# Performance work log

Hardware: AMD Instinct MI355X
Metric: run time of the kernel (lower is better)

## Reference

```python
import jax, jax.numpy as jnp
import numpy as np

B, S, D = 16, 4096, 128
LN_EPS = 1e-5
REC_EPS = 1e-8


def setup_inputs() -> dict:
    key = jax.random.key(0)
    k1, k2, k3, k4 = jax.random.split(key, 4)
    return {
        "C": jax.random.normal(k1, (B, S, D), dtype=jnp.float32),
        "V": jax.random.normal(k2, (B, S, D), dtype=jnp.float32),
        "W": jax.random.normal(k3, (B, S, D), dtype=jnp.float32),
        "encoder_context": jax.random.normal(k4, (B, D), dtype=jnp.float32),
        "time_modulation": jnp.full((1, 1, D), 0.5, dtype=jnp.float32),
        "context_modulation": jnp.full((1, D), 0.5, dtype=jnp.float32),
        "ln_weight": jnp.ones((D,), dtype=jnp.float32),
        "ln_bias": jnp.zeros((D,), dtype=jnp.float32),
    }


def reference(C, V, W, encoder_context, time_modulation, context_modulation, ln_weight, ln_bias):
    b_, s_, d_ = C.shape
    tm = time_modulation[0, 0]  # [D]
    # context gate is time-invariant: compute once
    ctx_add = jax.nn.sigmoid(encoder_context * context_modulation) * encoder_context  # [B,D]

    def step(carry, xs):
        a, bst = carry  # a: [B,1], bst: [B,D]
        c_t, v_t, w_t = xs  # each [B,D]
        decay = jax.nn.sigmoid(w_t * tm)  # [B,D]
        ec = jnp.exp(c_t)  # [B,D]
        a = decay.mean(axis=1, keepdims=True) * a + ec.sum(axis=1, keepdims=True)
        bst = decay * bst + ec * v_t + ctx_add
        out_t = bst / (a + REC_EPS)
        return (a, bst), out_t

    a0 = jnp.zeros((b_, 1), dtype=C.dtype)
    b0 = jnp.zeros((b_, d_), dtype=C.dtype)
    xs = (jnp.swapaxes(C, 0, 1), jnp.swapaxes(V, 0, 1), jnp.swapaxes(W, 0, 1))  # [S,B,D]
    _, ys = jax.lax.scan(step, (a0, b0), xs)  # ys: [S,B,D]
    res = jnp.swapaxes(ys, 0, 1)  # [B,S,D]

    mu = jnp.mean(res, axis=-1, keepdims=True)
    var = jnp.var(res, axis=-1, keepdims=True)
    normed = (res - mu) * jax.lax.rsqrt(var + LN_EPS)
    return normed * ln_weight + ln_bias
```

## Files before the change

### kernel.cpp

```cpp
#include <hip/hip_runtime.h>

#define BB   16
#define SS   4096
#define DD   128
#define NCH  256
#define TT   (SS / NCH)
#define WPB  4
#define NTHR 256

#define DT   16
#define SUBS 16
#define CPS  (NCH / SUBS)

#define LN_EPS  1e-5f
#define REC_EPS 1e-8f

__device__ __forceinline__ float fast_rcp(float x) { return __builtin_amdgcn_rcpf(x); }
__device__ __forceinline__ float sigm(float x) { return fast_rcp(1.0f + __expf(-x)); }

__device__ __forceinline__ unsigned pack2(float a, float b) {
    unsigned ua = (__float_as_uint(a) + 0x8000u) >> 16;
    unsigned ub = (__float_as_uint(b) + 0x8000u) & 0xFFFF0000u;
    return ub | ua;
}
__device__ __forceinline__ float up_lo(unsigned u) { return __uint_as_float(u << 16); }
__device__ __forceinline__ float up_hi(unsigned u) { return __uint_as_float(u & 0xFFFF0000u); }

template<int CTRL>
__device__ __forceinline__ float dpp_mov0(float x) {
    return __int_as_float(
        __builtin_amdgcn_update_dpp(0, __float_as_int(x), CTRL, 0xF, 0xF, true));
}

__device__ __forceinline__ void wave_red2(float& a, float& b) {
    a += dpp_mov0<0x111>(a); b += dpp_mov0<0x111>(b);
    a += dpp_mov0<0x112>(a); b += dpp_mov0<0x112>(b);
    a += dpp_mov0<0x114>(a); b += dpp_mov0<0x114>(b);
    a += dpp_mov0<0x118>(a); b += dpp_mov0<0x118>(b);
    a += dpp_mov0<0x142>(a); b += dpp_mov0<0x142>(b);
    a += dpp_mov0<0x143>(a); b += dpp_mov0<0x143>(b);
    a = __int_as_float(__builtin_amdgcn_readlane(__float_as_int(a), 63));
    b = __int_as_float(__builtin_amdgcn_readlane(__float_as_int(b), 63));
}

#define LOAD_FENCE() asm volatile("" ::: "memory")

__global__ __launch_bounds__(NTHR, 2) void pass1_kernel(
    const float* __restrict__ C, const float* __restrict__ V, const float* __restrict__ W,
    const float* __restrict__ enc, const float* __restrict__ tmod, const float* __restrict__ cmod,
    unsigned* __restrict__ DTb,
    float* __restrict__ Pbuf, float* __restrict__ Qbuf,
    float* __restrict__ PaBuf, float* __restrict__ QaBuf,
    float2* __restrict__ MEbuf)
{
    const int wv   = threadIdx.x >> 6;
    const int lane = threadIdx.x & 63;
    const int gc   = blockIdx.x * WPB + wv;
    const int b    = gc >> 8;
    const int ch   = gc & (NCH - 1);
    const int d2   = lane << 1;

    const int t0 = ch * TT;
    const size_t base = ((size_t)b * SS + t0) * DD + d2;
    const float2* Cp = (const float2*)(C + base);
    const float2* Vp = (const float2*)(V + base);
    const float2* Wp = (const float2*)(W + base);
    uint2* DTp = (uint2*)(DTb + base);

    const float2 tm = *(const float2*)(tmod + d2);
    const float2 cm = *(const float2*)(cmod + d2);
    const float2 ec = *(const float2*)(enc + b * DD + d2);

    float2 cR[TT], wR[TT], vR[TT];
#pragma unroll
    for (int t = 0; t < TT; ++t) {
        cR[t] = Cp[t * (DD / 2)];
        wR[t] = Wp[t * (DD / 2)];
        vR[t] = Vp[t * (DD / 2)];
    }
    LOAD_FENCE();

    float2 ctx;
    ctx.x = sigm(ec.x * cm.x) * ec.x;
    ctx.y = sigm(ec.y * cm.y) * ec.y;

    float2 P = make_float2(1.f, 1.f);
    float2 Q = make_float2(0.f, 0.f);
    float pa = 1.f, qa = 0.f;
    float mkeep = 0.f, ekeep = 0.f;

#pragma unroll
    for (int t = 0; t < TT; ++t) {
        float2 dec, e2, T2;
        dec.x = sigm(wR[t].x * tm.x); dec.y = sigm(wR[t].y * tm.y);
        e2.x = __expf(cR[t].x); e2.y = __expf(cR[t].y);
        T2.x = e2.x * vR[t].x + ctx.x;
        T2.y = e2.y * vR[t].y + ctx.y;

        uint2 u;
        u.x = pack2(dec.x, T2.x); u.y = pack2(dec.y, T2.y);
        DTp[t * (DD / 2)] = u;

        const float dqx = up_lo(u.x), dqy = up_lo(u.y);
        const float tqx = up_hi(u.x), tqy = up_hi(u.y);
        Q.x = dqx * Q.x + tqx;
        Q.y = dqy * Q.y + tqy;
        P.x *= dqx; P.y *= dqy;

        float sd = dec.x + dec.y;
        float se = e2.x + e2.y;
        wave_red2(sd, se);
        const float mt = sd * (1.0f / DD);
        pa *= mt;
        qa = mt * qa + se;
        if (lane == t) { mkeep = mt; ekeep = se; }
    }

    *(float2*)(Pbuf + (size_t)gc * DD + d2) = P;
    *(float2*)(Qbuf + (size_t)gc * DD + d2) = Q;
    if (lane < TT) MEbuf[(size_t)b * SS + t0 + lane] = make_float2(mkeep, ekeep);
    if (lane == 0) { PaBuf[gc] = pa; QaBuf[gc] = qa; }
}

__global__ __launch_bounds__(256) void pass2_kernel(
    const float* __restrict__ Pbuf, const float* __restrict__ Qbuf,
    const float* __restrict__ PaBuf, const float* __restrict__ QaBuf,
    float* __restrict__ bst0, float* __restrict__ a0)
{
    const int b   = blockIdx.x >> 3;
    const int dt  = blockIdx.x & 7;
    const int tid = threadIdx.x;
    const int dl  = tid & (DT - 1);
    const int sub = tid >> 4;
    const int d   = dt * DT + dl;

    __shared__ float cP[SUBS][DT], cQ[SUBS][DT], ent[SUBS][DT];
    __shared__ float sPa[NCH], sQa[NCH];

    const int ch0 = sub * CPS;
    const size_t base = ((size_t)b * NCH + ch0) * DD + d;
    float Pr[CPS], Qr[CPS];
    float p = 1.f, q = 0.f;
#pragma unroll
    for (int i = 0; i < CPS; ++i) {
        Pr[i] = Pbuf[base + (size_t)i * DD];
        Qr[i] = Qbuf[base + (size_t)i * DD];
        q = Pr[i] * q + Qr[i];
        p = Pr[i] * p;
    }
    cP[sub][dl] = p; cQ[sub][dl] = q;
    __syncthreads();

    if (tid < DT) {
        float s = 0.f;
#pragma unroll
        for (int sb = 0; sb < SUBS; ++sb) {
            ent[sb][tid] = s;
            s = cP[sb][tid] * s + cQ[sb][tid];
        }
    }
    __syncthreads();

    float s = ent[sub][dl];
#pragma unroll
    for (int i = 0; i < CPS; ++i) {
        bst0[base + (size_t)i * DD] = s;
        s = Pr[i] * s + Qr[i];
    }

    if (dt == 0) {
        float pa = PaBuf[b * NCH + tid];
        float qa = QaBuf[b * NCH + tid];
#pragma unroll
        for (int off = 1; off < NCH; off <<= 1) {
            sPa[tid] = pa; sQa[tid] = qa;
            __syncthreads();
            if (tid >= off) {
                const float pp = sPa[tid - off], qq = sQa[tid - off];
                qa = pa * qq + qa;
                pa = pa * pp;
            }
            __syncthreads();
        }
        sQa[tid] = qa;
        __syncthreads();
        a0[b * NCH + tid] = (tid == 0) ? 0.f : sQa[tid - 1];
    }
}

__global__ __launch_bounds__(NTHR, 4) void pass3_kernel(
    const unsigned* __restrict__ DTb,
    const float* __restrict__ lnw, const float* __restrict__ lnb,
    const float* __restrict__ bst0, const float* __restrict__ a0,
    const float2* __restrict__ MEbuf,
    float* __restrict__ out)
{
    const int wv   = threadIdx.x >> 6;
    const int lane = threadIdx.x & 63;
    const int gc   = blockIdx.x * WPB + wv;
    const int b    = gc >> 8;
    const int ch   = gc & (NCH - 1);
    const int d2   = lane << 1;

    const int t0 = ch * TT;
    const size_t base = ((size_t)b * SS + t0) * DD + d2;
    const uint2* DTp = (const uint2*)(DTb + base);
    float2* Op = (float2*)(out + base);

    uint2 dtR[TT];
#pragma unroll
    for (int t = 0; t < TT; ++t) dtR[t] = DTp[t * (DD / 2)];
    const float2 me = MEbuf[(size_t)b * SS + t0 + (lane & (TT - 1))];
    float2 bst = *(const float2*)(bst0 + (size_t)gc * DD + d2);
    const float a_in = a0[gc];
    const float2 gw = *(const float2*)(lnw + d2);
    const float2 gb = *(const float2*)(lnb + d2);
    LOAD_FENCE();

    float a = a_in;

#pragma unroll
    for (int t = 0; t < TT; ++t) {
        const float mt = __int_as_float(__builtin_amdgcn_readlane(__float_as_int(me.x), t));
        const float et = __int_as_float(__builtin_amdgcn_readlane(__float_as_int(me.y), t));

        a = mt * a + et;
        bst.x = up_lo(dtR[t].x) * bst.x + up_hi(dtR[t].x);
        bst.y = up_lo(dtR[t].y) * bst.y + up_hi(dtR[t].y);

        const float inva = fast_rcp(a + REC_EPS);
        float2 o;
        o.x = bst.x * inva; o.y = bst.y * inva;

        float s1 = o.x + o.y;
        float s2 = o.x * o.x + o.y * o.y;
        wave_red2(s1, s2);
        const float mu  = s1 * (1.0f / DD);
        const float var = s2 * (1.0f / DD) - mu * mu;
        const float rs  = rsqrtf(var + LN_EPS);

        float2 r;
        r.x = (o.x - mu) * rs * gw.x + gb.x;
        r.y = (o.y - mu) * rs * gw.y + gb.y;
        Op[t * (DD / 2)] = r;
    }
}

extern "C" void kernel_launch(void* const* d_in, const int* in_sizes, int n_in,
                              void* d_out, int out_size, void* d_ws, size_t ws_size,
                              hipStream_t stream)
{
    const float* C    = (const float*)d_in[0];
    const float* V    = (const float*)d_in[1];
    const float* W    = (const float*)d_in[2];
    const float* enc  = (const float*)d_in[3];
    const float* tmod = (const float*)d_in[4];
    const float* cmod = (const float*)d_in[5];
    const float* lnw  = (const float*)d_in[6];
    const float* lnb  = (const float*)d_in[7];
    float* out = (float*)d_out;

    float* ws    = (float*)d_ws;
    unsigned* DTbuf = (unsigned*)ws;
    float* Pbuf  = ws    + (size_t)BB * SS * DD;
    float* Qbuf  = Pbuf  + (size_t)BB * NCH * DD;
    float* bst0  = Qbuf  + (size_t)BB * NCH * DD;
    float2* MEbuf = (float2*)(bst0 + (size_t)BB * NCH * DD);
    float* PaBuf = (float*)(MEbuf + (size_t)BB * SS);
    float* QaBuf = PaBuf + (size_t)BB * NCH;
    float* a0Buf = QaBuf + (size_t)BB * NCH;

    const int nblk = BB * NCH / WPB;
    pass1_kernel<<<nblk, NTHR, 0, stream>>>(C, V, W, enc, tmod, cmod, DTbuf,
                                            Pbuf, Qbuf, PaBuf, QaBuf, MEbuf);
    pass2_kernel<<<BB * 8, 256, 0, stream>>>(Pbuf, Qbuf, PaBuf, QaBuf, bst0, a0Buf);
    pass3_kernel<<<nblk, NTHR, 0, stream>>>(DTbuf, lnw, lnb,
                                            bst0, a0Buf, MEbuf, out);
}
```

Measured before the change: 160.6 us.

## Double chunk count and batch wave reductions out of the serial time loops

Raises the number of sequence chunks from 256 to 512, so each wave handles 8 timesteps instead of 16, and raises occupancy hints on pass1 and pass2. In pass1 and pass3 the per-timestep cross-lane DPP reductions are pulled out of the serial recurrence into a separate batched loop, so independent reductions can interleave instead of serializing with the scan. The pass2 scalar scan now combines two chunks per thread so a 256-thread block still covers 512 chunks. The aim is more parallelism and better latency hiding, at the cost of more chunk-carry traffic and more live registers.

After: 157.8 us, median of 2. Within noise of the previous version (-1.8%).

```diff
diff --git a/kernel.cpp b/kernel.cpp
--- a/kernel.cpp
+++ b/kernel.cpp
@@ -3,14 +3,14 @@
 #define BB   16
 #define SS   4096
 #define DD   128
-#define NCH  256
+#define NCH  512
 #define TT   (SS / NCH)
 #define WPB  4
 #define NTHR 256
 
-#define DT   16
-#define SUBS 16
-#define CPS  (NCH / SUBS)
+#define DTILE 16
+#define SUBS  16
+#define CPS   (NCH / SUBS)
 
 #define LN_EPS  1e-5f
 #define REC_EPS 1e-8f
@@ -45,7 +45,7 @@
 
 #define LOAD_FENCE() asm volatile("" ::: "memory")
 
-__global__ __launch_bounds__(NTHR, 2) void pass1_kernel(
+__global__ __launch_bounds__(NTHR, 4) void pass1_kernel(
     const float* __restrict__ C, const float* __restrict__ V, const float* __restrict__ W,
     const float* __restrict__ enc, const float* __restrict__ tmod, const float* __restrict__ cmod,
     unsigned* __restrict__ DTb,
@@ -56,7 +56,7 @@
     const int wv   = threadIdx.x >> 6;
     const int lane = threadIdx.x & 63;
     const int gc   = blockIdx.x * WPB + wv;
-    const int b    = gc >> 8;
+    const int b    = gc >> 9;
     const int ch   = gc & (NCH - 1);
     const int d2   = lane << 1;
 
@@ -86,18 +86,16 @@
 
     float2 P = make_float2(1.f, 1.f);
     float2 Q = make_float2(0.f, 0.f);
-    float pa = 1.f, qa = 0.f;
-    float mkeep = 0.f, ekeep = 0.f;
-
-#pragma unroll
-    for (int t = 0; t < TT; ++t) {
-        float2 dec, e2, T2;
+    float sdp[TT], sep[TT];
+
+#pragma unroll
+    for (int t = 0; t < TT; ++t) {
+        float2 dec, e2, T2; uint2 u;
         dec.x = sigm(wR[t].x * tm.x); dec.y = sigm(wR[t].y * tm.y);
         e2.x = __expf(cR[t].x); e2.y = __expf(cR[t].y);
         T2.x = e2.x * vR[t].x + ctx.x;
         T2.y = e2.y * vR[t].y + ctx.y;
 
-        uint2 u;
         u.x = pack2(dec.x, T2.x); u.y = pack2(dec.y, T2.y);
         DTp[t * (DD / 2)] = u;
 
@@ -107,22 +105,30 @@
         Q.y = dqy * Q.y + tqy;
         P.x *= dqx; P.y *= dqy;
 
-        float sd = dec.x + dec.y;
-        float se = e2.x + e2.y;
-        wave_red2(sd, se);
-        const float mt = sd * (1.0f / DD);
+        sdp[t] = dec.x + dec.y;
+        sep[t] = e2.x + e2.y;
+    }
+
+#pragma unroll
+    for (int t = 0; t < TT; ++t) wave_red2(sdp[t], sep[t]);
+
+    float pa = 1.f, qa = 0.f;
+    float mk = 0.f, ek = 0.f;
+#pragma unroll
+    for (int t = 0; t < TT; ++t) {
+        const float mt = sdp[t] * (1.0f / DD);
         pa *= mt;
-        qa = mt * qa + se;
-        if (lane == t) { mkeep = mt; ekeep = se; }
+        qa = mt * qa + sep[t];
+        if (lane == t) { mk = mt; ek = sep[t]; }
     }
 
     *(float2*)(Pbuf + (size_t)gc * DD + d2) = P;
     *(float2*)(Qbuf + (size_t)gc * DD + d2) = Q;
-    if (lane < TT) MEbuf[(size_t)b * SS + t0 + lane] = make_float2(mkeep, ekeep);
+    if (lane < TT) MEbuf[(size_t)b * SS + t0 + lane] = make_float2(mk, ek);
     if (lane == 0) { PaBuf[gc] = pa; QaBuf[gc] = qa; }
 }
 
-__global__ __launch_bounds__(256) void pass2_kernel(
+__global__ __launch_bounds__(256, 2) void pass2_kernel(
     const float* __restrict__ Pbuf, const float* __restrict__ Qbuf,
     const float* __restrict__ PaBuf, const float* __restrict__ QaBuf,
     float* __restrict__ bst0, float* __restrict__ a0)
@@ -130,12 +136,12 @@
     const int b   = blockIdx.x >> 3;
     const int dt  = blockIdx.x & 7;
     const int tid = threadIdx.x;
-    const int dl  = tid & (DT - 1);
+    const int dl  = tid & (DTILE - 1);
     const int sub = tid >> 4;
-    const int d   = dt * DT + dl;
-
-    __shared__ float cP[SUBS][DT], cQ[SUBS][DT], ent[SUBS][DT];
-    __shared__ float sPa[NCH], sQa[NCH];
+    const int d   = dt * DTILE + dl;
+
+    __shared__ float cP[SUBS][DTILE], cQ[SUBS][DTILE], ent[SUBS][DTILE];
+    __shared__ float sPa[256], sQa[256];
 
     const int ch0 = sub * CPS;
     const size_t base = ((size_t)b * NCH + ch0) * DD + d;
@@ -151,7 +157,7 @@
     cP[sub][dl] = p; cQ[sub][dl] = q;
     __syncthreads();
 
-    if (tid < DT) {
+    if (tid < DTILE) {
         float s = 0.f;
 #pragma unroll
         for (int sb = 0; sb < SUBS; ++sb) {
@@ -169,22 +175,27 @@
     }
 
     if (dt == 0) {
-        float pa = PaBuf[b * NCH + tid];
-        float qa = QaBuf[b * NCH + tid];
-#pragma unroll
-        for (int off = 1; off < NCH; off <<= 1) {
-            sPa[tid] = pa; sQa[tid] = qa;
+        const int cbase = b * NCH;
+        const float p0 = PaBuf[cbase + 2 * tid],     q0 = QaBuf[cbase + 2 * tid];
+        const float p1 = PaBuf[cbase + 2 * tid + 1], q1 = QaBuf[cbase + 2 * tid + 1];
+        float Pc = p1 * p0;
+        float Qc = p1 * q0 + q1;
+#pragma unroll
+        for (int off = 1; off < 256; off <<= 1) {
+            sPa[tid] = Pc; sQa[tid] = Qc;
             __syncthreads();
             if (tid >= off) {
                 const float pp = sPa[tid - off], qq = sQa[tid - off];
-                qa = pa * qq + qa;
-                pa = pa * pp;
+                Qc = Pc * qq + Qc;
+                Pc = Pc * pp;
             }
             __syncthreads();
         }
-        sQa[tid] = qa;
+        sQa[tid] = Qc;
         __syncthreads();
-        a0[b * NCH + tid] = (tid == 0) ? 0.f : sQa[tid - 1];
+        const float E = (tid == 0) ? 0.f : sQa[tid - 1];
+        a0[cbase + 2 * tid]     = E;
+        a0[cbase + 2 * tid + 1] = p0 * E + q0;
     }
 }
 
@@ -198,7 +209,7 @@
     const int wv   = threadIdx.x >> 6;
     const int lane = threadIdx.x & 63;
     const int gc   = blockIdx.x * WPB + wv;
-    const int b    = gc >> 8;
+    const int b    = gc >> 9;
     const int ch   = gc & (NCH - 1);
     const int d2   = lane << 1;
 
@@ -218,7 +229,8 @@
     LOAD_FENCE();
 
     float a = a_in;
-
+    float2 o[TT];
+    float s1p[TT], s2p[TT];
 #pragma unroll
     for (int t = 0; t < TT; ++t) {
         const float mt = __int_as_float(__builtin_amdgcn_readlane(__float_as_int(me.x), t));
@@ -229,19 +241,22 @@
         bst.y = up_lo(dtR[t].y) * bst.y + up_hi(dtR[t].y);
 
         const float inva = fast_rcp(a + REC_EPS);
-        float2 o;
-        o.x = bst.x * inva; o.y = bst.y * inva;
-
-        float s1 = o.x + o.y;
-        float s2 = o.x * o.x + o.y * o.y;
-        wave_red2(s1, s2);
-        const float mu  = s1 * (1.0f / DD);
-        const float var = s2 * (1.0f / DD) - mu * mu;
+        o[t].x = bst.x * inva; o[t].y = bst.y * inva;
+        s1p[t] = o[t].x + o[t].y;
+        s2p[t] = o[t].x * o[t].x + o[t].y * o[t].y;
+    }
+
+#pragma unroll
+    for (int t = 0; t < TT; ++t) wave_red2(s1p[t], s2p[t]);
+
+#pragma unroll
+    for (int t = 0; t < TT; ++t) {
+        const float mu  = s1p[t] * (1.0f / DD);
+        const float var = s2p[t] * (1.0f / DD) - mu * mu;
         const float rs  = rsqrtf(var + LN_EPS);
-
         float2 r;
-        r.x = (o.x - mu) * rs * gw.x + gb.x;
-        r.y = (o.y - mu) * rs * gw.y + gb.y;
+        r.x = (o[t].x - mu) * rs * gw.x + gb.x;
+        r.y = (o[t].y - mu) * rs * gw.y + gb.y;
         Op[t * (DD / 2)] = r;
     }
 }
```
